# Kernel tuning notes

Measured on AMD Instinct MI355X. Metric: run time of the kernel, lower is better.

Reference implementation:

```python
import jax, jax.numpy as jnp
import numpy as np

EPS = 1e-5


def gcn_conv(x, src, dst, n_nodes, W, b):
    # x: [B, N, Fin]; src/dst: [E+N] (self loops included); W: [Fout, Fin]
    h = jnp.einsum('bnf,of->bno', x, W)                      # [B, N, Fout]
    deg = jnp.zeros((n_nodes,), h.dtype).at[dst].add(1.0)    # in-degree of A+I
    dinv = jnp.where(deg > 0, 1.0 / jnp.sqrt(deg), 0.0)
    norm = dinv[src] * dinv[dst]                             # [E+N]
    msg = h[:, src, :] * norm[None, :, None]                 # gather along node axis
    out = jnp.zeros_like(h).at[:, dst, :].add(msg)           # scatter-add aggregate
    return out + b


def batchnorm_nodes(x, gamma, beta):
    # torch BatchNorm1d(N) on [B, N, C]: channel axis is N, stats over (B, C)
    mean = jnp.mean(x, axis=(0, 2), keepdims=True)
    var = jnp.mean(jnp.square(x - mean), axis=(0, 2), keepdims=True)
    xn = (x - mean) * jax.lax.rsqrt(var + EPS)
    return xn * gamma[None, :, None] + beta[None, :, None]


def setup_inputs() -> dict:
    key = jax.random.key(0)
    ks = jax.random.split(key, 20)
    B, N, FIN, D, OUT, E = 4096, 64, 67, 2048, 2, 512
    s = 0.1
    d = {}
    d['x_fingerprints'] = jax.random.normal(ks[0], (B, D), jnp.float32)
    d['x_node_features'] = jax.random.normal(ks[1], (B, N, FIN), jnp.float32)
    d['edge_list'] = jax.random.randint(ks[2], (2, E), 0, N)
    d['W1'] = jax.random.normal(ks[3], (64, FIN), jnp.float32) * s
    d['b1'] = jax.random.normal(ks[4], (64,), jnp.float32) * s
    d['g1'] = 1.0 + jax.random.normal(ks[5], (N,), jnp.float32) * s
    d['be1'] = jax.random.normal(ks[6], (N,), jnp.float32) * s
    d['W2'] = jax.random.normal(ks[7], (32, 64), jnp.float32) * s
    d['b2'] = jax.random.normal(ks[8], (32,), jnp.float32) * s
    d['g2'] = 1.0 + jax.random.normal(ks[9], (N,), jnp.float32) * s
    d['be2'] = jax.random.normal(ks[10], (N,), jnp.float32) * s
    d['Wl1'] = jax.random.normal(ks[11], (400, D), jnp.float32) * (s / 4)
    d['bl1'] = jax.random.normal(ks[12], (400,), jnp.float32) * s
    d['Wl2'] = jax.random.normal(ks[13], (64, 400), jnp.float32) * s
    d['bl2'] = jax.random.normal(ks[14], (64,), jnp.float32) * s
    d['Wfc'] = jax.random.normal(ks[15], (OUT, 96), jnp.float32) * s
    d['bfc'] = jax.random.normal(ks[16], (OUT,), jnp.float32) * s
    return d


def reference(x_fingerprints, x_node_features, edge_list, W1, b1, g1, be1,
              W2, b2, g2, be2, Wl1, bl1, Wl2, bl2, Wfc, bfc):
    B, N, _ = x_node_features.shape
    loops = jnp.arange(N)
    src = jnp.concatenate([edge_list[0], loops])  # add self loops (GCNConv default)
    dst = jnp.concatenate([edge_list[1], loops])
    g = gcn_conv(x_node_features, src, dst, N, W1, b1)
    g = jax.nn.relu(batchnorm_nodes(g, g1, be1))
    g = gcn_conv(g, src, dst, N, W2, b2)
    g = jax.nn.relu(batchnorm_nodes(g, g2, be2))           # [B, N, 32]
    pooled = jnp.max(g, axis=1)                             # global_max_pool -> [B, 32]
    h = jax.nn.relu(x_fingerprints @ Wl1.T + bl1)
    h = jax.nn.relu(h @ Wl2.T + bl2)                        # [B, 64]
    out = jnp.concatenate([pooled, h], axis=1) @ Wfc.T + bfc
    return out
```

## Files before the change

### kernel.cpp

```cpp
#include <hip/hip_runtime.h>
#include <hip/hip_bf16.h>
#include <math.h>

typedef __bf16 bf16;
typedef __attribute__((ext_vector_type(8))) __bf16 bf16x8;
typedef __attribute__((ext_vector_type(4))) __bf16 bf16x4;
typedef __attribute__((ext_vector_type(4))) float f32x4;

#define EPSBN 1e-5f
#define B_    4096
#define N_    64
#define FIN_  67
#define E_    512
#define NSLOT 128

__device__ inline bf16x8 pack8(f32x4 lo, f32x4 hi) {
    bf16x8 r;
    r[0] = (bf16)lo[0]; r[1] = (bf16)lo[1]; r[2] = (bf16)lo[2]; r[3] = (bf16)lo[3];
    r[4] = (bf16)hi[0]; r[5] = (bf16)hi[1]; r[6] = (bf16)hi[2]; r[7] = (bf16)hi[3];
    return r;
}

__global__ __launch_bounds__(256) void k0_prep(const int* __restrict__ edge,
    const float* __restrict__ W1, const float* __restrict__ W2,
    float* __restrict__ partials,
    bf16* __restrict__ an_hi, bf16* __restrict__ an_lo,
    bf16* __restrict__ wpad,
    bf16* __restrict__ w2pad)
{
    int tid = threadIdx.x;
    for (int i = blockIdx.x * 256 + tid; i < NSLOT * 64 * 4; i += gridDim.x * 256)
        partials[i] = 0.f;
    if (blockIdx.x == 1) {
        for (int i = tid; i < 64 * 104; i += 256) {
            int n = i / 104, f = i % 104;
            wpad[i] = (f < FIN_) ? (bf16)W1[n * FIN_ + f] : (bf16)0.f;
        }
        return;
    }
    if (blockIdx.x == 2) {
        for (int i = tid; i < 32 * 72; i += 256) {
            int o = i / 72, f = i % 72;
            w2pad[i] = (f < 64) ? (bf16)W2[o * 64 + f] : (bf16)0.f;
        }
        return;
    }
    if (blockIdx.x != 0) return;

    __shared__ float An[64 * 64];
    __shared__ int ssrc[E_], sdst[E_];
    __shared__ int deg[N_];
    __shared__ float dinv[N_];
    for (int i = tid; i < 64 * 64; i += 256) An[i] = 0.f;
    for (int i = tid; i < E_; i += 256) { ssrc[i] = edge[i]; sdst[i] = edge[E_ + i]; }
    if (tid < N_) deg[tid] = 1;
    __syncthreads();
    for (int i = tid; i < E_; i += 256) atomicAdd(&deg[sdst[i]], 1);
    __syncthreads();
    if (tid < N_) dinv[tid] = rsqrtf((float)deg[tid]);
    __syncthreads();
    for (int i = tid; i < E_; i += 256) {
        int s = ssrc[i], d = sdst[i];
        atomicAdd(&An[d * 64 + s], dinv[s] * dinv[d]);
    }
    if (tid < N_) atomicAdd(&An[tid * 64 + tid], dinv[tid] * dinv[tid]);
    __syncthreads();
    for (int i = tid; i < 64 * 64; i += 256) {
        float v = An[i];
        bf16 h = (bf16)v;
        an_hi[i] = h;
        an_lo[i] = (bf16)(v - (float)h);
    }
}

__global__ __launch_bounds__(256, 3) void k1_gcn1(
    const float* __restrict__ x,
    const float* __restrict__ b1,
    const bf16* __restrict__ an_hi, const bf16* __restrict__ an_lo,
    const bf16* __restrict__ wpad,
    bf16* __restrict__ g1out,
    float* __restrict__ part1)
{
    __shared__ union {
        float xraw[4352];
        struct { bf16 hhi[64 * 72]; bf16 hlo[64 * 72]; } h;
    } u;
    __shared__ bf16 ost[64 * 72];

    int tid = threadIdx.x;
    int w = tid >> 6, lane = tid & 63, q = lane >> 4, r15 = lane & 15;
    int arow = w * 16 + r15;

    bf16x8 wf[3][4];
#pragma unroll
    for (int kt = 0; kt < 3; ++kt)
#pragma unroll
        for (int nt = 0; nt < 4; ++nt)
            wf[kt][nt] = *(const bf16x8*)&wpad[(nt * 16 + r15) * 104 + kt * 32 + q * 8];

    const bf16* ahp = an_hi + arow * 64 + q * 8;
    const bf16* alp = an_lo + arow * 64 + q * 8;
    bf16x8 Ah0 = *(const bf16x8*)ahp;
    bf16x8 Ah1 = *(const bf16x8*)(ahp + 32);
    bf16x8 Al0 = *(const bf16x8*)alp;
    bf16x8 Al1 = *(const bf16x8*)(alp + 32);

    float bc[4];
#pragma unroll
    for (int nt = 0; nt < 4; ++nt) bc[nt] = b1[nt * 16 + r15];

    size_t b0 = (size_t)blockIdx.x * 4;
    const f32x4* xb4 = (const f32x4*)(x + b0 * 4288);

    f32x4 pre0 = xb4[tid], pre1 = xb4[tid + 256], pre2 = xb4[tid + 512], pre3 = xb4[tid + 768];
    f32x4 pre4 = {0.f, 0.f, 0.f, 0.f};
    if (tid < 48) pre4 = xb4[tid + 1024];

    f32x4* xl4 = (f32x4*)u.xraw;
    f32x4 z4 = {0.f, 0.f, 0.f, 0.f};

#pragma unroll 1
    for (int g = 0; g < 4; ++g) {
        int b = (int)b0 + g;
        xl4[tid] = pre0; xl4[tid + 256] = pre1; xl4[tid + 512] = pre2; xl4[tid + 768] = pre3;
        if (tid < 48) xl4[tid + 1024] = pre4;
        __syncthreads();

        f32x4 acc[4] = {z4, z4, z4, z4};
        const float* xr = u.xraw + arow * FIN_;
#pragma unroll
        for (int kt = 0; kt < 3; ++kt) {
            bf16x8 a;
            if (kt < 2) {
                int k0 = kt * 32 + q * 8;
#pragma unroll
                for (int j = 0; j < 8; ++j) a[j] = (bf16)xr[k0 + j];
            } else {
#pragma unroll
                for (int j = 0; j < 8; ++j) a[j] = (bf16)0.f;
                if (q == 0) { a[0] = (bf16)xr[64]; a[1] = (bf16)xr[65]; a[2] = (bf16)xr[66]; }
            }
#pragma unroll
            for (int nt = 0; nt < 4; ++nt)
                acc[nt] = __builtin_amdgcn_mfma_f32_16x16x32_bf16(a, wf[kt][nt], acc[nt], 0, 0, 0);
        }
        if (g < 3) {
            const f32x4* xn = xb4 + (size_t)(g + 1) * 1072;
            pre0 = xn[tid]; pre1 = xn[tid + 256]; pre2 = xn[tid + 512]; pre3 = xn[tid + 768];
            if (tid < 48) pre4 = xn[tid + 1024];
        }
        __syncthreads();

        int sbase = w * 16 + q * 4;
#pragma unroll
        for (int nt = 0; nt < 4; ++nt) {
            int c = nt * 16 + r15;
            bf16x4 hi, lo;
#pragma unroll
            for (int r = 0; r < 4; ++r) {
                float v = acc[nt][r];
                bf16 h = (bf16)v;
                hi[r] = h; lo[r] = (bf16)(v - (float)h);
            }
            *(bf16x4*)&u.h.hhi[c * 72 + sbase] = hi;
            *(bf16x4*)&u.h.hlo[c * 72 + sbase] = lo;
        }
        __syncthreads();

        f32x4 acc2[4] = {z4, z4, z4, z4};
#pragma unroll
        for (int kt = 0; kt < 2; ++kt) {
            bf16x8 Ahk = kt ? Ah1 : Ah0;
            bf16x8 Alk = kt ? Al1 : Al0;
#pragma unroll
            for (int nt = 0; nt < 4; ++nt) {
                int o = (nt * 16 + r15) * 72 + kt * 32 + q * 8;
                bf16x8 Hh = *(const bf16x8*)&u.h.hhi[o];
                bf16x8 Hl = *(const bf16x8*)&u.h.hlo[o];
                acc2[nt] = __builtin_amdgcn_mfma_f32_16x16x32_bf16(Ahk, Hh, acc2[nt], 0, 0, 0);
                acc2[nt] = __builtin_amdgcn_mfma_f32_16x16x32_bf16(Ahk, Hl, acc2[nt], 0, 0, 0);
                acc2[nt] = __builtin_amdgcn_mfma_f32_16x16x32_bf16(Alk, Hh, acc2[nt], 0, 0, 0);
            }
        }
#pragma unroll
        for (int nt = 0; nt < 4; ++nt) {
            int c = nt * 16 + r15;
#pragma unroll
            for (int r = 0; r < 4; ++r)
                ost[(sbase + r) * 72 + c] = (bf16)(acc2[nt][r] + bc[nt]);
        }
        __syncthreads();

        int n = tid >> 2, oq = tid & 3;
        bf16x8 o0 = *(const bf16x8*)&ost[n * 72 + oq * 16];
        bf16x8 o1 = *(const bf16x8*)&ost[n * 72 + oq * 16 + 8];
        bf16* gp = g1out + ((size_t)b * 4096 + n * 64 + oq * 16);
        *(bf16x8*)gp = o0;
        *(bf16x8*)(gp + 8) = o1;
        float s1 = 0.f, s2 = 0.f;
#pragma unroll
        for (int j = 0; j < 8; ++j) {
            float v0 = (float)o0[j], v1 = (float)o1[j];
            s1 += v0 + v1; s2 += v0 * v0 + v1 * v1;
        }
        s1 += __shfl_xor(s1, 1); s1 += __shfl_xor(s1, 2);
        s2 += __shfl_xor(s2, 1); s2 += __shfl_xor(s2, 2);
        if (oq == 0) {
            int slot = b & (NSLOT - 1);
            atomicAdd(&part1[(slot * 64 + n) * 2 + 0], s1);
            atomicAdd(&part1[(slot * 64 + n) * 2 + 1], s2);
        }
    }
}

__global__ __launch_bounds__(64) void k_bnstats(
    const float* __restrict__ part,
    const float* __restrict__ gamma, const float* __restrict__ beta,
    float* __restrict__ scale, float* __restrict__ shift, float inv_count)
{
    int n = blockIdx.x, t = threadIdx.x;
    float s1 = part[(t * 64 + n) * 2] + part[((t + 64) * 64 + n) * 2];
    float s2 = part[(t * 64 + n) * 2 + 1] + part[((t + 64) * 64 + n) * 2 + 1];
#pragma unroll
    for (int o = 32; o > 0; o >>= 1) { s1 += __shfl_down(s1, o); s2 += __shfl_down(s2, o); }
    if (t == 0) {
        float mean = s1 * inv_count;
        float var = s2 * inv_count - mean * mean;
        float sc = gamma[n] * rsqrtf(var + EPSBN);
        scale[n] = sc;
        shift[n] = beta[n] - mean * sc;
    }
}

__global__ __launch_bounds__(256, 4) void k3_gcn2(
    const bf16* __restrict__ g1out,
    const float* __restrict__ b2,
    const float* __restrict__ scale1, const float* __restrict__ shift1,
    const bf16* __restrict__ an_hi, const bf16* __restrict__ an_lo,
    const bf16* __restrict__ w2pad,
    bf16* __restrict__ g2out,
    float* __restrict__ part2)
{
    __shared__ bf16 ya[64 * 72];
    __shared__ bf16 hhi[32 * 72];
    __shared__ bf16 hlo[32 * 72];
    __shared__ bf16 ost[64 * 40];

    int tid = threadIdx.x;
    int w = tid >> 6, lane = tid & 63, q = lane >> 4, r15 = lane & 15;
    int arow = w * 16 + r15;

    bf16x8 wf[2][2];
#pragma unroll
    for (int kt = 0; kt < 2; ++kt)
#pragma unroll
        for (int nt = 0; nt < 2; ++nt)
            wf[kt][nt] = *(const bf16x8*)&w2pad[(nt * 16 + r15) * 72 + kt * 32 + q * 8];

    const bf16* ahp = an_hi + arow * 64 + q * 8;
    const bf16* alp = an_lo + arow * 64 + q * 8;
    bf16x8 Ah0 = *(const bf16x8*)ahp;
    bf16x8 Ah1 = *(const bf16x8*)(ahp + 32);
    bf16x8 Al0 = *(const bf16x8*)alp;
    bf16x8 Al1 = *(const bf16x8*)(alp + 32);
    float sc = scale1[arow], sh = shift1[arow];
    float bc[2] = { b2[r15], b2[16 + r15] };

    size_t b0 = (size_t)blockIdx.x * 4;
    const bf16x8* gg8 = (const bf16x8*)(g1out + b0 * 4096);
    bf16x8 p0 = gg8[tid], p1 = gg8[tid + 256];

    int r0 = tid >> 3, c0 = (tid & 7) * 8;
    f32x4 z4 = {0.f, 0.f, 0.f, 0.f};

#pragma unroll 1
    for (int g = 0; g < 4; ++g) {
        int b = (int)b0 + g;
        *(bf16x8*)&ya[r0 * 72 + c0] = p0;
        *(bf16x8*)&ya[(r0 + 32) * 72 + c0] = p1;
        __syncthreads();

        f32x4 acc[2] = {z4, z4};
#pragma unroll
        for (int kt = 0; kt < 2; ++kt) {
            int k0 = kt * 32 + q * 8;
            bf16x8 raw = *(const bf16x8*)&ya[arow * 72 + k0];
            bf16x8 a;
#pragma unroll
            for (int j = 0; j < 8; ++j)
                a[j] = (bf16)fmaxf(fmaf(sc, (float)raw[j], sh), 0.f);
#pragma unroll
            for (int nt = 0; nt < 2; ++nt)
                acc[nt] = __builtin_amdgcn_mfma_f32_16x16x32_bf16(a, wf[kt][nt], acc[nt], 0, 0, 0);
        }
        if (g < 3) {
            p0 = gg8[(size_t)(g + 1) * 512 + tid];
            p1 = gg8[(size_t)(g + 1) * 512 + tid + 256];
        }
        __syncthreads();

        int sbase = w * 16 + q * 4;
#pragma unroll
        for (int nt = 0; nt < 2; ++nt) {
            int c = nt * 16 + r15;
            bf16x4 hi, lo;
#pragma unroll
            for (int r = 0; r < 4; ++r) {
                float v = acc[nt][r];
                bf16 h = (bf16)v;
                hi[r] = h; lo[r] = (bf16)(v - (float)h);
            }
            *(bf16x4*)&hhi[c * 72 + sbase] = hi;
            *(bf16x4*)&hlo[c * 72 + sbase] = lo;
        }
        __syncthreads();

        f32x4 acc2[2] = {z4, z4};
#pragma unroll
        for (int kt = 0; kt < 2; ++kt) {
            bf16x8 Ahk = kt ? Ah1 : Ah0;
            bf16x8 Alk = kt ? Al1 : Al0;
#pragma unroll
            for (int nt = 0; nt < 2; ++nt) {
                int o = (nt * 16 + r15) * 72 + kt * 32 + q * 8;
                bf16x8 Hh = *(const bf16x8*)&hhi[o];
                bf16x8 Hl = *(const bf16x8*)&hlo[o];
                acc2[nt] = __builtin_amdgcn_mfma_f32_16x16x32_bf16(Ahk, Hh, acc2[nt], 0, 0, 0);
                acc2[nt] = __builtin_amdgcn_mfma_f32_16x16x32_bf16(Ahk, Hl, acc2[nt], 0, 0, 0);
                acc2[nt] = __builtin_amdgcn_mfma_f32_16x16x32_bf16(Alk, Hh, acc2[nt], 0, 0, 0);
            }
        }
#pragma unroll
        for (int nt = 0; nt < 2; ++nt) {
            int c = nt * 16 + r15;
#pragma unroll
            for (int r = 0; r < 4; ++r)
                ost[(sbase + r) * 40 + c] = (bf16)(acc2[nt][r] + bc[nt]);
        }
        __syncthreads();

        int n = tid >> 2, oq = tid & 3;
        bf16x8 ov = *(const bf16x8*)&ost[n * 40 + oq * 8];
        *(bf16x8*)(g2out + ((size_t)b * 2048 + n * 32 + oq * 8)) = ov;
        float s1 = 0.f, s2 = 0.f;
#pragma unroll
        for (int j = 0; j < 8; ++j) {
            float v = (float)ov[j];
            s1 += v; s2 += v * v;
        }
        s1 += __shfl_xor(s1, 1); s1 += __shfl_xor(s1, 2);
        s2 += __shfl_xor(s2, 1); s2 += __shfl_xor(s2, 2);
        if (oq == 0) {
            int slot = b & (NSLOT - 1);
            atomicAdd(&part2[(slot * 64 + n) * 2 + 0], s1);
            atomicAdd(&part2[(slot * 64 + n) * 2 + 1], s2);
        }
    }
}

__global__ __launch_bounds__(256) void k6_mlp1(
    const float* __restrict__ A,
    const float* __restrict__ Bw,
    float* __restrict__ part)
{
    __shared__ bf16 As[64 * 36];
    __shared__ bf16 Bs[64 * 36];
    int tid = threadIdx.x;
    int m0 = blockIdx.x * 64, n0 = blockIdx.y * 64, ks = blockIdx.z;
    int row = tid >> 2, seg = tid & 3;
    int w = tid >> 6, lane = tid & 63, q = lane >> 4, r15 = lane & 15;
    f32x4 z4 = {0.f, 0.f, 0.f, 0.f};
    f32x4 acc[4] = {z4, z4, z4, z4};
    const float* pA = A + (size_t)(m0 + row) * 2048 + ks * 512 + seg * 8;
    bool bvalid = (n0 + row) < 400;
    const float* pB = Bw + (size_t)(n0 + row) * 2048 + ks * 512 + seg * 8;

    f32x4 a[2][2], c[2][2];
    c[0][0] = z4; c[0][1] = z4; c[1][0] = z4; c[1][1] = z4;

#define LD(s, t)                                                              \
    do {                                                                      \
        const float* _a = pA + (t) * 32;                                      \
        a[s][0] = *(const f32x4*)_a; a[s][1] = *(const f32x4*)(_a + 4);       \
        if (bvalid) {                                                         \
            const float* _b = pB + (t) * 32;                                  \
            c[s][0] = *(const f32x4*)_b; c[s][1] = *(const f32x4*)(_b + 4);   \
        }                                                                     \
    } while (0)

    LD(0, 0);
    LD(1, 1);

#pragma unroll
    for (int kt = 0; kt < 16; ++kt) {
        const int sl = kt & 1;
        bf16x8 apk = pack8(a[sl][0], a[sl][1]);
        bf16x8 bpk = pack8(c[sl][0], c[sl][1]);
        __syncthreads();
        *(bf16x8*)&As[row * 36 + seg * 8] = apk;
        *(bf16x8*)&Bs[row * 36 + seg * 8] = bpk;
        __syncthreads();
        if (kt < 14) LD(sl, kt + 2);
        bf16x8 af = *(const bf16x8*)&As[(w * 16 + r15) * 36 + q * 8];
#pragma unroll
        for (int nt = 0; nt < 4; ++nt) {
            bf16x8 bb = *(const bf16x8*)&Bs[(nt * 16 + r15) * 36 + q * 8];
            acc[nt] = __builtin_amdgcn_mfma_f32_16x16x32_bf16(af, bb, acc[nt], 0, 0, 0);
        }
    }
#undef LD

    float* pp = part + (size_t)ks * 1638400;
#pragma unroll
    for (int nt = 0; nt < 4; ++nt)
#pragma unroll
        for (int r = 0; r < 4; ++r) {
            int mm = m0 + w * 16 + q * 4 + r;
            int nn = n0 + nt * 16 + r15;
            if (nn < 400) pp[(size_t)mm * 400 + nn] = acc[nt][r];
        }
}

__global__ __launch_bounds__(256) void k7_mlp2(
    const float* __restrict__ part,
    const float* __restrict__ bl1,
    const float* __restrict__ Bw,
    const float* __restrict__ bias,
    float* __restrict__ Cout)
{
    __shared__ bf16 As[16 * 416];
    int tid = threadIdx.x;
    int m0 = blockIdx.x * 16;
    for (int i = tid; i < 800; i += 256) {
        int rr = i / 50, cc = (i % 50) * 8;
        const float* p0 = part + (size_t)(m0 + rr) * 400 + cc;
        f32x4 x0 = *(const f32x4*)p0,             x1 = *(const f32x4*)(p0 + 4);
        f32x4 y0 = *(const f32x4*)(p0 + 1638400), y1 = *(const f32x4*)(p0 + 1638404);
        f32x4 u0 = *(const f32x4*)(p0 + 3276800), u1 = *(const f32x4*)(p0 + 3276804);
        f32x4 v0 = *(const f32x4*)(p0 + 4915200), v1 = *(const f32x4*)(p0 + 4915204);
        f32x4 w0 = *(const f32x4*)&bl1[cc],       w1 = *(const f32x4*)&bl1[cc + 4];
        bf16x8 o;
#pragma unroll
        for (int j = 0; j < 4; ++j) {
            o[j]     = (bf16)fmaxf(x0[j] + y0[j] + u0[j] + v0[j] + w0[j], 0.f);
            o[4 + j] = (bf16)fmaxf(x1[j] + y1[j] + u1[j] + v1[j] + w1[j], 0.f);
        }
        *(bf16x8*)&As[rr * 416 + cc] = o;
    }
    if (tid < 32) {
        int rr = tid >> 1, cc = 400 + (tid & 1) * 8;
        bf16x8 z;
#pragma unroll
        for (int k = 0; k < 8; ++k) z[k] = (bf16)0.f;
        *(bf16x8*)&As[rr * 416 + cc] = z;
    }
    __syncthreads();

    int w = tid >> 6, lane = tid & 63, q = lane >> 4, r15 = lane & 15;
    f32x4 acc = {0.f, 0.f, 0.f, 0.f};
    const float* pB = Bw + (size_t)(w * 16 + r15) * 400;
#pragma unroll 4
    for (int kt = 0; kt < 13; ++kt) {
        int k0 = kt * 32 + q * 8;
        bf16x8 a = *(const bf16x8*)&As[r15 * 416 + k0];
        bf16x8 bb;
#pragma unroll
        for (int k = 0; k < 8; ++k) bb[k] = (bf16)0.f;
        if (k0 < 400) {
            f32x4 c0 = *(const f32x4*)(pB + k0);
            f32x4 c1 = *(const f32x4*)(pB + k0 + 4);
            bb[0] = (bf16)c0[0]; bb[1] = (bf16)c0[1]; bb[2] = (bf16)c0[2]; bb[3] = (bf16)c0[3];
            bb[4] = (bf16)c1[0]; bb[5] = (bf16)c1[1]; bb[6] = (bf16)c1[2]; bb[7] = (bf16)c1[3];
        }
        acc = __builtin_amdgcn_mfma_f32_16x16x32_bf16(a, bb, acc, 0, 0, 0);
    }
#pragma unroll
    for (int r = 0; r < 4; ++r) {
        int mm = m0 + q * 4 + r;
        int nn = w * 16 + r15;
        float v = fmaxf(acc[r] + bias[nn], 0.f);
        Cout[(size_t)mm * 64 + nn] = v;
    }
}

__global__ __launch_bounds__(256) void k8_final(
    const bf16* __restrict__ g2out,
    const float* __restrict__ scale2, const float* __restrict__ shift2,
    const float* __restrict__ h2,
    const float* __restrict__ Wfc,
    const float* __restrict__ bfc,
    float* __restrict__ out)
{
    __shared__ float s2s[64], sh2s[64];
    int tid = threadIdx.x;
    if (tid < 64) { s2s[tid] = scale2[tid]; sh2s[tid] = shift2[tid]; }
    __syncthreads();
    int w = tid >> 6, lane = tid & 63;
    int b = blockIdx.x * 4 + w;
    int c = lane & 31, half = lane >> 5;
    const bf16* gb = g2out + (size_t)b * 2048;
    float mx = 0.f;
    for (int i = 0; i < 32; ++i) {
        int n = half * 32 + i;
        float v = (float)gb[n * 32 + c];
        float val = fmaf(s2s[n], v, sh2s[n]);
        mx = fmaxf(mx, val);
    }
    mx = fmaxf(mx, __shfl_xor(mx, 32));
    float h2v = h2[(size_t)b * 64 + lane];
#pragma unroll
    for (int o = 0; o < 2; ++o) {
        float t = h2v * Wfc[o * 96 + 32 + lane];
        if (half == 0) t += mx * Wfc[o * 96 + c];
#pragma unroll
        for (int off = 32; off > 0; off >>= 1) t += __shfl_xor(t, off);
        if (lane == 0) out[(size_t)b * 2 + o] = t + bfc[o];
    }
}

extern "C" void kernel_launch(void* const* d_in, const int* in_sizes, int n_in,
                              void* d_out, int out_size, void* d_ws, size_t ws_size,
                              hipStream_t stream)
{
    const float* x_fp   = (const float*)d_in[0];
    const float* x_node = (const float*)d_in[1];
    const int*   edge   = (const int*)d_in[2];
    const float* W1     = (const float*)d_in[3];
    const float* b1     = (const float*)d_in[4];
    const float* g1     = (const float*)d_in[5];
    const float* be1    = (const float*)d_in[6];
    const float* W2     = (const float*)d_in[7];
    const float* b2     = (const float*)d_in[8];
    const float* g2     = (const float*)d_in[9];
    const float* be2    = (const float*)d_in[10];
    const float* Wl1    = (const float*)d_in[11];
    const float* bl1    = (const float*)d_in[12];
    const float* Wl2    = (const float*)d_in[13];
    const float* bl2    = (const float*)d_in[14];
    const float* Wfc    = (const float*)d_in[15];
    const float* bfc    = (const float*)d_in[16];
    float* out = (float*)d_out;

    char* ws = (char*)d_ws;
    float* scale1  = (float*)(ws + 5632);
    float* shift1  = (float*)(ws + 5888);
    float* scale2  = (float*)(ws + 6144);
    float* shift2  = (float*)(ws + 6400);
    float* part1   = (float*)(ws + 8192);
    float* part2   = (float*)(ws + 8192 + 65536);
    bf16*  g1out   = (bf16*)(ws + 139264);
    float* part6   = (float*)(ws + 139264);
    bf16*  g2out   = (bf16*)(ws + 33693696ull);
    float* h2      = (float*)(ws + 53747712ull);
    bf16*  an_hi   = (bf16*)(ws + 53747712ull);
    bf16*  an_lo   = (bf16*)(ws + 53747712ull + 8192);
    bf16*  wpad    = (bf16*)(ws + 53747712ull + 16384);
    bf16*  w2pad   = (bf16*)(ws + 53747712ull + 32768);

    k0_prep<<<dim3(64), dim3(256), 0, stream>>>(edge, W1, W2, part1, an_hi, an_lo, wpad, w2pad);
    k1_gcn1<<<dim3(1024), dim3(256), 0, stream>>>(x_node, b1, an_hi, an_lo, wpad, g1out, part1);
    k_bnstats<<<dim3(64), dim3(64), 0, stream>>>(part1, g1, be1, scale1, shift1,
                                                 1.f / (4096.f * 64.f));
    k3_gcn2<<<dim3(1024), dim3(256), 0, stream>>>(g1out, b2, scale1, shift1,
                                                  an_hi, an_lo, w2pad, g2out, part2);
    k_bnstats<<<dim3(64), dim3(64), 0, stream>>>(part2, g2, be2, scale2, shift2,
                                                 1.f / (4096.f * 32.f));
    k6_mlp1<<<dim3(64, 7, 4), dim3(256), 0, stream>>>(x_fp, Wl1, part6);
    k7_mlp2<<<dim3(256), dim3(256), 0, stream>>>(part6, bl1, Wl2, bl2, h2);
    k8_final<<<dim3(1024), dim3(256), 0, stream>>>(g2out, scale2, shift2, h2, Wfc, bfc, out);
}
```

Baseline: 246.1 us.

## Pre-convert Wl1 to padded bf16 and load MLP1 fragments directly from global

The prep kernel now also converts Wl1 to bf16, zero-padded to 448 rows, in workspace. The first MLP GEMM drops its LDS staging and both block barriers, and each wave loads its A and B MFMA fragments straight from global memory with a two-stage register double buffer. This removes the per-iteration barriers, LDS traffic and B-side fp32 conversion, but B rows are now fetched redundantly by all four waves and A is read with a less coalesced per-lane pattern.

```diff
diff --git a/kernel.cpp b/kernel.cpp
--- a/kernel.cpp
+++ b/kernel.cpp
@@ -23,10 +23,12 @@
 
 __global__ __launch_bounds__(256) void k0_prep(const int* __restrict__ edge,
     const float* __restrict__ W1, const float* __restrict__ W2,
+    const float* __restrict__ Wl1,
     float* __restrict__ partials,
     bf16* __restrict__ an_hi, bf16* __restrict__ an_lo,
     bf16* __restrict__ wpad,
-    bf16* __restrict__ w2pad)
+    bf16* __restrict__ w2pad,
+    bf16* __restrict__ wl1b)
 {
     int tid = threadIdx.x;
     for (int i = blockIdx.x * 256 + tid; i < NSLOT * 64 * 4; i += gridDim.x * 256)
@@ -45,7 +47,21 @@
         }
         return;
     }
-    if (blockIdx.x != 0) return;
+    if (blockIdx.x >= 3) {
+        for (int i = (blockIdx.x - 3) * 256 + tid; i < 448 * 256; i += 61 * 256) {
+            int row = i >> 8, col = (i & 255) * 8;
+            bf16x8 o;
+            if (row < 400) {
+                const float* p = Wl1 + (size_t)row * 2048 + col;
+                o = pack8(*(const f32x4*)p, *(const f32x4*)(p + 4));
+            } else {
+#pragma unroll
+                for (int k = 0; k < 8; ++k) o[k] = (bf16)0.f;
+            }
+            *(bf16x8*)&wl1b[(size_t)row * 2048 + col] = o;
+        }
+        return;
+    }
 
     __shared__ float An[64 * 64];
     __shared__ int ssrc[E_], sdst[E_];
@@ -360,65 +376,66 @@
 
 __global__ __launch_bounds__(256) void k6_mlp1(
     const float* __restrict__ A,
-    const float* __restrict__ Bw,
+    const bf16* __restrict__ Bw,
     float* __restrict__ part)
 {
-    __shared__ bf16 As[64 * 36];
-    __shared__ bf16 Bs[64 * 36];
     int tid = threadIdx.x;
     int m0 = blockIdx.x * 64, n0 = blockIdx.y * 64, ks = blockIdx.z;
-    int row = tid >> 2, seg = tid & 3;
     int w = tid >> 6, lane = tid & 63, q = lane >> 4, r15 = lane & 15;
     f32x4 z4 = {0.f, 0.f, 0.f, 0.f};
     f32x4 acc[4] = {z4, z4, z4, z4};
-    const float* pA = A + (size_t)(m0 + row) * 2048 + ks * 512 + seg * 8;
-    bool bvalid = (n0 + row) < 400;
-    const float* pB = Bw + (size_t)(n0 + row) * 2048 + ks * 512 + seg * 8;
-
-    f32x4 a[2][2], c[2][2];
-    c[0][0] = z4; c[0][1] = z4; c[1][0] = z4; c[1][1] = z4;
-
-#define LD(s, t)                                                              \
-    do {                                                                      \
-        const float* _a = pA + (t) * 32;                                      \
-        a[s][0] = *(const f32x4*)_a; a[s][1] = *(const f32x4*)(_a + 4);       \
-        if (bvalid) {                                                         \
-            const float* _b = pB + (t) * 32;                                  \
-            c[s][0] = *(const f32x4*)_b; c[s][1] = *(const f32x4*)(_b + 4);   \
-        }                                                                     \
+
+    const float* pA = A + (size_t)(m0 + w * 16 + r15) * 2048 + ks * 512 + q * 8;
+    const bf16* pB0 = Bw + (size_t)(n0 + r15) * 2048 + ks * 512 + q * 8;
+    const bf16* pB1 = pB0 + 16 * 2048;
+    const bf16* pB2 = pB0 + 32 * 2048;
+    const bf16* pB3 = pB0 + 48 * 2048;
+
+    f32x4 aA0, aA1, bA0, bA1;
+    bf16x8 aB0, aB1, aB2, aB3, bB0, bB1, bB2, bB3;
+
+#define LD0(t) do { \
+        aA0 = *(const f32x4*)(pA + (t) * 32); aA1 = *(const f32x4*)(pA + (t) * 32 + 4); \
+        aB0 = *(const bf16x8*)(pB0 + (t) * 32); aB1 = *(const bf16x8*)(pB1 + (t) * 32); \
+        aB2 = *(const bf16x8*)(pB2 + (t) * 32); aB3 = *(const bf16x8*)(pB3 + (t) * 32); \
     } while (0)
-
-    LD(0, 0);
-    LD(1, 1);
-
-#pragma unroll
-    for (int kt = 0; kt < 16; ++kt) {
-        const int sl = kt & 1;
-        bf16x8 apk = pack8(a[sl][0], a[sl][1]);
-        bf16x8 bpk = pack8(c[sl][0], c[sl][1]);
-        __syncthreads();
-        *(bf16x8*)&As[row * 36 + seg * 8] = apk;
-        *(bf16x8*)&Bs[row * 36 + seg * 8] = bpk;
-        __syncthreads();
-        if (kt < 14) LD(sl, kt + 2);
-        bf16x8 af = *(const bf16x8*)&As[(w * 16 + r15) * 36 + q * 8];
-#pragma unroll
-        for (int nt = 0; nt < 4; ++nt) {
-            bf16x8 bb = *(const bf16x8*)&Bs[(nt * 16 + r15) * 36 + q * 8];
-            acc[nt] = __builtin_amdgcn_mfma_f32_16x16x32_bf16(af, bb, acc[nt], 0, 0, 0);
-        }
-    }
-#undef LD
+#define LD1(t) do { \
+        bA0 = *(const f32x4*)(pA + (t) * 32); bA1 = *(const f32x4*)(pA + (t) * 32 + 4); \
+        bB0 = *(const bf16x8*)(pB0 + (t) * 32); bB1 = *(const bf16x8*)(pB1 + (t) * 32); \
+        bB2 = *(const bf16x8*)(pB2 + (t) * 32); bB3 = *(const bf16x8*)(pB3 + (t) * 32); \
+    } while (0)
+
+    LD0(0); LD1(1);
+#pragma unroll
+    for (int t = 0; t < 16; t += 2) {
+        bf16x8 af0 = pack8(aA0, aA1);
+        acc[0] = __builtin_amdgcn_mfma_f32_16x16x32_bf16(af0, aB0, acc[0], 0, 0, 0);
+        acc[1] = __builtin_amdgcn_mfma_f32_16x16x32_bf16(af0, aB1, acc[1], 0, 0, 0);
+        acc[2] = __builtin_amdgcn_mfma_f32_16x16x32_bf16(af0, aB2, acc[2], 0, 0, 0);
+        acc[3] = __builtin_amdgcn_mfma_f32_16x16x32_bf16(af0, aB3, acc[3], 0, 0, 0);
+        if (t + 2 < 16) LD0(t + 2);
+        bf16x8 af1 = pack8(bA0, bA1);
+        acc[0] = __builtin_amdgcn_mfma_f32_16x16x32_bf16(af1, bB0, acc[0], 0, 0, 0);
+        acc[1] = __builtin_amdgcn_mfma_f32_16x16x32_bf16(af1, bB1, acc[1], 0, 0, 0);
+        acc[2] = __builtin_amdgcn_mfma_f32_16x16x32_bf16(af1, bB2, acc[2], 0, 0, 0);
+        acc[3] = __builtin_amdgcn_mfma_f32_16x16x32_bf16(af1, bB3, acc[3], 0, 0, 0);
+        if (t + 3 < 16) LD1(t + 3);
+    }
+#undef LD0
+#undef LD1
 
     float* pp = part + (size_t)ks * 1638400;
 #pragma unroll
-    for (int nt = 0; nt < 4; ++nt)
-#pragma unroll
-        for (int r = 0; r < 4; ++r) {
-            int mm = m0 + w * 16 + q * 4 + r;
-            int nn = n0 + nt * 16 + r15;
-            if (nn < 400) pp[(size_t)mm * 400 + nn] = acc[nt][r];
-        }
+    for (int nt = 0; nt < 4; ++nt) {
+        int nn = n0 + nt * 16 + r15;
+        if (nn < 400) {
+#pragma unroll
+            for (int r = 0; r < 4; ++r) {
+                int mm = m0 + w * 16 + q * 4 + r;
+                pp[(size_t)mm * 400 + nn] = acc[nt][r];
+            }
+        }
+    }
 }
 
 __global__ __launch_bounds__(256) void k7_mlp2(
@@ -556,8 +573,10 @@
     bf16*  an_lo   = (bf16*)(ws + 53747712ull + 8192);
     bf16*  wpad    = (bf16*)(ws + 53747712ull + 16384);
     bf16*  w2pad   = (bf16*)(ws + 53747712ull + 32768);
-
-    k0_prep<<<dim3(64), dim3(256), 0, stream>>>(edge, W1, W2, part1, an_hi, an_lo, wpad, w2pad);
+    bf16*  wl1b    = (bf16*)(ws + 58720256ull);
+
+    k0_prep<<<dim3(64), dim3(256), 0, stream>>>(edge, W1, W2, Wl1, part1,
+                                                an_hi, an_lo, wpad, w2pad, wl1b);
     k1_gcn1<<<dim3(1024), dim3(256), 0, stream>>>(x_node, b1, an_hi, an_lo, wpad, g1out, part1);
     k_bnstats<<<dim3(64), dim3(64), 0, stream>>>(part1, g1, be1, scale1, shift1,
                                                  1.f / (4096.f * 64.f));
@@ -565,7 +584,7 @@
                                                   an_hi, an_lo, w2pad, g2out, part2);
     k_bnstats<<<dim3(64), dim3(64), 0, stream>>>(part2, g2, be2, scale2, shift2,
                                                  1.f / (4096.f * 32.f));
-    k6_mlp1<<<dim3(64, 7, 4), dim3(256), 0, stream>>>(x_fp, Wl1, part6);
+    k6_mlp1<<<dim3(64, 7, 4), dim3(256), 0, stream>>>(x_fp, wl1b, part6);
     k7_mlp2<<<dim3(256), dim3(256), 0, stream>>>(part6, bl1, Wl2, bl2, h2);
     k8_final<<<dim3(1024), dim3(256), 0, stream>>>(g2out, scale2, shift2, h2, Wfc, bfc, out);
 }
```

Measured after the change: 286.3 us. +16.3%, slower.
